# Kernel optimization log

Hardware: AMD Instinct MI355X
Metric: run time of the kernel (lower is better)

## Reference

```python
import jax, jax.numpy as jnp
import numpy as np

N = 20000
T = 6890
FEAT = 128
DEG = 32
K = 6


def setup_inputs() -> dict:
    key = jax.random.key(0)
    k1, k2, k3, k4, k5 = jax.random.split(key, 5)
    source_feats = jax.random.normal(k1, (N, FEAT), dtype=jnp.float32)
    target_feats = jax.random.normal(k2, (T, FEAT), dtype=jnp.float32)
    target_points = jax.random.normal(k3, (T, 3), dtype=jnp.float32)
    pos = jax.random.normal(k4, (N, 3), dtype=jnp.float32)
    # kNN-style graph: every center node (row) has exactly DEG neighbors (col)
    row = jnp.repeat(jnp.arange(N, dtype=jnp.int32), DEG)
    col = jax.random.randint(k5, (N * DEG,), 0, N, dtype=jnp.int32)
    edge_index = jnp.stack([row, col], axis=0)  # [2, E]
    return {"source_feats": source_feats, "target_feats": target_feats,
            "target_points": target_points, "pos": pos, "edge_index": edge_index}


def reference(source_feats, target_feats, target_points, pos, edge_index):
    n = source_feats.shape[0]
    # --- soft retrieval against template ---
    dp = source_feats @ target_feats.T                                 # [N,T]
    dists = ((source_feats * source_feats).sum(-1, keepdims=True)
             - 2.0 * dp
             + (target_feats * target_feats).sum(-1)[None, :])         # [N,T]
    neg_scores, indices = jax.lax.top_k(-dists, K)                      # [N,K]
    scores = jax.nn.softmax(neg_scores, axis=-1)                        # [N,K]
    selected = target_points[indices]                                   # [N,K,3]
    predicted = (selected * scores[..., None]).sum(-2)                  # [N,3]

    row, col = edge_index[0], edge_index[1]
    src_nb = pos[col]                                                   # [E,3]
    tgt_nb = predicted[col]                                             # [E,3]

    cnt = jax.ops.segment_sum(jnp.ones(row.shape, src_nb.dtype), row,
                              num_segments=n)
    cnt = jnp.maximum(cnt, 1.0)[:, None]                                # [N,1]
    src_centers = jax.ops.segment_sum(src_nb, row, num_segments=n) / cnt
    tgt_centers = jax.ops.segment_sum(tgt_nb, row, num_segments=n) / cnt

    sd = src_nb - src_centers[row]                                      # [E,3]
    td = tgt_nb - tgt_centers[row]                                      # [E,3]
    edge_mat = sd[:, :, None] * td[:, None, :]                          # [E,3,3] outer products
    pm = jax.ops.segment_sum(edge_mat, row, num_segments=n)             # [N,3,3]

    # --- Procrustes via batched 3x3 SVD (torch.svd: A = U S V^T; jnp: A = U S Vh => V^T = Vh) ---
    U, S, Vh = jnp.linalg.svd(pm)
    R0 = jax.lax.stop_gradient(U @ Vh)
    detR0 = jnp.linalg.det(R0)
    d = jax.lax.stop_gradient(
        jnp.stack([jnp.ones_like(detR0), jnp.ones_like(detR0), detR0], -1))  # [N,3]
    R = (U * d[:, None, :]) @ Vh                                        # U @ diag(d) @ V^T
    trans = tgt_centers - jnp.einsum('nij,nj->ni', R, src_centers)      # [N,3]

    # --- residual under neighbor transforms ---
    transformed = jnp.einsum('eij,ej->ei', R[col], src_nb) + trans[col]  # [E,3]
    res = transformed - tgt_nb
    dsts = (res * res).sum(-1, keepdims=True)                           # [E,1]
    dst = jax.ops.segment_sum(dsts, row, num_segments=n) / cnt          # [N,1]
    return R, trans, dst
```

## Files before the change

### kernel.cpp

```cpp
#include <hip/hip_runtime.h>
#include <math.h>

#define NS 20000
#define TT 6890
#define TPAD 6912
#define FE 128
#define EDG 640000
#define DEG 32

#define RPB 80
#define NCB 4
#define CBW 1728
#define NH 5

typedef __attribute__((ext_vector_type(8))) short short8;
typedef __attribute__((ext_vector_type(4))) float floatx4;
typedef __attribute__((ext_vector_type(4))) int i32x4;
typedef unsigned int uint;

__device__ __forceinline__ unsigned short f2bf(float f) {
  unsigned int u = __float_as_uint(f);
  return (unsigned short)((u + 0x7fffu + ((u >> 16) & 1u)) >> 16);
}

__device__ __forceinline__ uint med3u(uint a, uint b, uint c) {
  uint d;
  asm("v_med3_u32 %0, %1, %2, %3" : "=v"(d) : "v"(a), "v"(b), "v"(c));
  return d;
}
__device__ __forceinline__ void ins6(uint* a, uint t) {
  a[5] = med3u(a[4], a[5], t);
  a[4] = med3u(a[3], a[4], t);
  a[3] = med3u(a[2], a[3], t);
  a[2] = med3u(a[1], a[2], t);
  a[1] = med3u(a[0], a[1], t);
  a[0] = min(a[0], t);
}
__device__ __forceinline__ void ins12(uint* a, uint t) {
  a[11] = med3u(a[10], a[11], t);
  a[10] = med3u(a[9], a[10], t);
  a[9]  = med3u(a[8], a[9], t);
  a[8]  = med3u(a[7], a[8], t);
  a[7]  = med3u(a[6], a[7], t);
  a[6]  = med3u(a[5], a[6], t);
  a[5]  = med3u(a[4], a[5], t);
  a[4]  = med3u(a[3], a[4], t);
  a[3]  = med3u(a[2], a[3], t);
  a[2]  = med3u(a[1], a[2], t);
  a[1]  = med3u(a[0], a[1], t);
  a[0]  = min(a[0], t);
}

__global__ void tn_cast_kernel(const float* __restrict__ tf, float* __restrict__ tn,
                               float* __restrict__ tn256,
                               unsigned short* __restrict__ tfbx) {
  int gid = blockIdx.x * blockDim.x + threadIdx.x;
  int w = gid >> 6;
  int lane = gid & 63;
  if (w >= TPAD) return;
  unsigned short* base = tfbx + (size_t)w * 128;
  int jj = lane >> 2;
  int soff = ((jj ^ (w & 7)) << 3) + (lane & 3) * 2;
  if (w < TT) {
    const float* p = tf + (size_t)w * FE;
    float a = p[lane];
    float b = p[lane + 64];
    float s = a * a + b * b;
#pragma unroll
    for (int off = 32; off > 0; off >>= 1) s += __shfl_xor(s, off);
    if (lane == 0) { tn[w] = s; tn256[w] = -0.5f * (s + 256.0f); }
    ushort2 o;
    o.x = f2bf(p[2 * lane]);
    o.y = f2bf(p[2 * lane + 1]);
    *reinterpret_cast<ushort2*>(base + soff) = o;
  } else {
    if (lane == 0) { tn[w] = 1e30f; tn256[w] = -1.5e38f; }
    ushort2 z; z.x = 0; z.y = 0;
    *reinterpret_cast<ushort2*>(base + soff) = z;
  }
}

union SmemK1 {
  unsigned short Bs[RPB * 128];
  uint pk[RPB][24];
};

__device__ __forceinline__ void mfma4_sel(
    short8 a0, short8 a1, short8 a2, short8 a3,
    short8 b0, short8 b1, short8 b2, short8 b3,
    float4 t4, uint ck, uint* kqh) {
  floatx4 acc = (floatx4){t4.x, t4.y, t4.z, t4.w};
  acc = __builtin_amdgcn_mfma_f32_16x16x32_bf16(a0, b0, acc, 0, 0, 0);
  acc = __builtin_amdgcn_mfma_f32_16x16x32_bf16(a1, b1, acc, 0, 0, 0);
  acc = __builtin_amdgcn_mfma_f32_16x16x32_bf16(a2, b2, acc, 0, 0, 0);
  acc = __builtin_amdgcn_mfma_f32_16x16x32_bf16(a3, b3, acc, 0, 0, 0);
#pragma unroll
  for (int r = 0; r < 4; ++r) {
    uint t = (__float_as_uint(acc[r]) & 0xFFFFE000u) | (ck + (uint)r);
    ins6(kqh, t);
  }
}

__global__ __launch_bounds__(256, 2) void topk_kernel(
    const float* __restrict__ sf, const unsigned short* __restrict__ tfbx,
    const float* __restrict__ tn256, uint* __restrict__ pkall) {
  __shared__ SmemK1 u;
  const int tid = threadIdx.x;
  const int lane = tid & 63;
  const int wv = tid >> 6;
  const int q = lane >> 4;
  const int m = lane & 15;
  const int rb = (int)blockIdx.x >> 2;
  const int cb = (int)blockIdx.x & 3;
  const int row0 = rb * RPB;
  const int cbase = cb * CBW;

#pragma unroll
  for (int t = 0; t < 5; ++t) {
    int c = tid + t * 256;
    int rr = c >> 4, jj = c & 15;
    const float* src = sf + (size_t)(row0 + rr) * FE + jj * 8;
    float4 f0 = *reinterpret_cast<const float4*>(src);
    float4 f1 = *reinterpret_cast<const float4*>(src + 4);
    union { unsigned short us[8]; uint4 v; } tt;
    tt.us[0] = f2bf(f0.x); tt.us[1] = f2bf(f0.y);
    tt.us[2] = f2bf(f0.z); tt.us[3] = f2bf(f0.w);
    tt.us[4] = f2bf(f1.x); tt.us[5] = f2bf(f1.y);
    tt.us[6] = f2bf(f1.z); tt.us[7] = f2bf(f1.w);
    *reinterpret_cast<uint4*>(u.Bs + rr * 128 + ((jj ^ (rr & 7)) << 3)) = tt.v;
  }

  uint kq[NH][6];
#pragma unroll
  for (int h = 0; h < NH; ++h)
#pragma unroll
    for (int k = 0; k < 6; ++k) kq[h][k] = 0xFFFFFFFFu;

  int rdB[4];
  int aoff[4];
  const int ax = m & 7;
#pragma unroll
  for (int ks = 0; ks < 4; ++ks) {
    int slot = (ks * 4 + q) ^ ax;
    rdB[ks] = m * 128 + (slot << 3);
    aoff[ks] = slot << 3;
  }
  const unsigned short* abase = tfbx + (size_t)(cbase + wv * 16 + m) * 128;
  const uint ck0 = (uint)(cbase + wv * 16 + q * 4);

  __syncthreads();

  short8 bf[NH][4];
  {
    uint bs0 = (uint)(uintptr_t)(&u.Bs[0]);
    uint adr[4];
#pragma unroll
    for (int ks = 0; ks < 4; ++ks) adr[ks] = bs0 + (uint)(rdB[ks] * 2);
#pragma unroll
    for (int h = 0; h < NH; ++h) {
#pragma unroll
      for (int ks = 0; ks < 4; ++ks) {
        union { i32x4 i; short8 s; } t;
        asm volatile("ds_read_b128 %0, %1 offset:%2"
                     : "=v"(t.i) : "v"(adr[ks]), "i"(h * 4096));
        bf[h][ks] = t.s;
      }
    }
    asm volatile("s_waitcnt lgkmcnt(0)" ::: "memory");
    __builtin_amdgcn_sched_barrier(0);
  }

  short8 a0 = *reinterpret_cast<const short8*>(abase + aoff[0]);
  short8 a1 = *reinterpret_cast<const short8*>(abase + aoff[1]);
  short8 a2 = *reinterpret_cast<const short8*>(abase + aoff[2]);
  short8 a3 = *reinterpret_cast<const short8*>(abase + aoff[3]);
  float4 t4 = *reinterpret_cast<const float4*>(tn256 + cbase + wv * 16 + q * 4);

  for (int s = 0; s < 27; ++s) {
    const int sn = (s < 26) ? s + 1 : 26;
    const unsigned short* apn = abase + (size_t)sn * 8192;
    short8 na0 = *reinterpret_cast<const short8*>(apn + aoff[0]);
    short8 na1 = *reinterpret_cast<const short8*>(apn + aoff[1]);
    short8 na2 = *reinterpret_cast<const short8*>(apn + aoff[2]);
    short8 na3 = *reinterpret_cast<const short8*>(apn + aoff[3]);
    float4 nt4 = *reinterpret_cast<const float4*>(
        tn256 + cbase + sn * 64 + wv * 16 + q * 4);
    const uint ck = ck0 + (uint)(s * 64);
#pragma unroll
    for (int h = 0; h < NH; ++h)
      mfma4_sel(a0, a1, a2, a3, bf[h][0], bf[h][1], bf[h][2], bf[h][3],
                t4, ck, kq[h]);
    a0 = na0; a1 = na1; a2 = na2; a3 = na3; t4 = nt4;
  }

#pragma unroll
  for (int h = 0; h < NH; ++h) {
#pragma unroll
    for (int st = 16; st <= 32; st <<= 1) {
      uint inc[6];
#pragma unroll
      for (int k = 0; k < 6; ++k) inc[k] = __shfl_xor(kq[h][k], st);
#pragma unroll
      for (int k = 0; k < 6; ++k) ins6(kq[h], inc[k]);
    }
  }
  __syncthreads();
  if (q == 0) {
#pragma unroll
    for (int h = 0; h < NH; ++h)
#pragma unroll
      for (int k = 0; k < 6; ++k) u.pk[h * 16 + m][wv * 6 + k] = kq[h][k];
  }
  __syncthreads();

  if (tid < RPB) {
    uint md[12];
#pragma unroll
    for (int k = 0; k < 12; ++k) md[k] = 0xFFFFFFFFu;
    for (int j = 0; j < 24; ++j) ins12(md, u.pk[tid][j]);
    uint* dst = pkall + (size_t)(row0 + tid) * 48 + cb * 12;
#pragma unroll
    for (int k = 0; k < 12; ++k) dst[k] = md[k];
  }
}

__global__ __launch_bounds__(256) void merge_kernel(
    const float* __restrict__ sf, const float* __restrict__ tf,
    const float* __restrict__ tn, const uint* __restrict__ pkall,
    const float* __restrict__ tp, float* __restrict__ pred) {
  __shared__ uint  kk[4][24];
  __shared__ float sv[4][24];
  __shared__ int   sc[4][24];
  const int lane = threadIdx.x & 63;
  const int wv = threadIdx.x >> 6;
  const int row = (int)blockIdx.x * 4 + wv;
  uint k0 = 0xFFFFFFFFu;
  if (lane < 48) k0 = pkall[(size_t)row * 48 + lane];
  int r0 = 0;
  for (int j = 0; j < 48; ++j) {
    uint a = __shfl(k0, j);
    r0 += (a < k0) ? 1 : 0;
  }
  if (lane < 48 && r0 < 24) kk[wv][r0] = k0;
  __syncthreads();

  const int g = lane >> 2;
  const int c4 = lane & 3;
  float4 sfc[8];
  const float* srow = sf + (size_t)row * FE;
#pragma unroll
  for (int it = 0; it < 8; ++it)
    sfc[it] = *reinterpret_cast<const float4*>(srow + (it * 4 + c4) * 4);
#pragma unroll
  for (int p = 0; p < 2; ++p) {
    const int j = p * 16 + g;
    if (j < 24) {
      const int col = (int)(kk[wv][j] & 0x1FFFu);
      const float* trow = tf + (size_t)col * FE;
      float acc = 0.f;
#pragma unroll
      for (int it = 0; it < 8; ++it) {
        float4 bv = *reinterpret_cast<const float4*>(trow + (it * 4 + c4) * 4);
        float4 av = sfc[it];
        acc += av.x * bv.x + av.y * bv.y + av.z * bv.z + av.w * bv.w;
      }
      acc += __shfl_xor(acc, 1);
      acc += __shfl_xor(acc, 2);
      if (c4 == 0) {
        sv[wv][j] = tn[col] - 2.f * acc;
        sc[wv][j] = col;
      }
    }
  }
  __syncthreads();
  if (lane == 0) {
    float sd[6]; int sp6[6];
#pragma unroll
    for (int k = 0; k < 6; ++k) { sd[k] = 1e30f; sp6[k] = 0; }
    for (int j = 0; j < 24; ++j) {
      float v = sv[wv][j];
      if (v < sd[5]) {
        sd[5] = v; sp6[5] = j;
#pragma unroll
        for (int k = 4; k >= 0; --k) {
          if (sd[k + 1] < sd[k]) {
            float tvv = sd[k]; sd[k] = sd[k + 1]; sd[k + 1] = tvv;
            int tii = sp6[k]; sp6[k] = sp6[k + 1]; sp6[k + 1] = tii;
          }
        }
      }
    }
    float wgt[6]; float wsum = 0.f;
#pragma unroll
    for (int k = 0; k < 6; ++k) { wgt[k] = __expf(sd[0] - sd[k]); wsum += wgt[k]; }
    float inv = 1.f / wsum;
    float px = 0.f, py = 0.f, pz = 0.f;
#pragma unroll
    for (int k = 0; k < 6; ++k) {
      float scv = wgt[k] * inv;
      const float* qq = tp + (size_t)sc[wv][sp6[k]] * 3;
      px += scv * qq[0]; py += scv * qq[1]; pz += scv * qq[2];
    }
    pred[row * 3 + 0] = px;
    pred[row * 3 + 1] = py;
    pred[row * 3 + 2] = pz;
  }
}

__global__ __launch_bounds__(256) void proc_kernel(
    const int* __restrict__ colp, const float* __restrict__ pos,
    const float* __restrict__ pred, float* __restrict__ Rout,
    float* __restrict__ tout, float* __restrict__ qnorm) {
  int t = blockIdx.x * blockDim.x + threadIdx.x;
  int i = t >> 2;
  int l = t & 3;
  if (i >= NS) return;
  int4 cia[2];
#pragma unroll
  for (int tt = 0; tt < 2; ++tt)
    cia[tt] = reinterpret_cast<const int4*>(colp + (size_t)i * DEG + l * 8)[tt];
  const int* cidx = reinterpret_cast<const int*>(cia);

  double sp[3] = {0, 0, 0}, sq[3] = {0, 0, 0};
  double spq[3][3] = {{0, 0, 0}, {0, 0, 0}, {0, 0, 0}};
#pragma unroll
  for (int e = 0; e < 8; ++e) {
    int c = cidx[e];
    double p0 = pos[c * 3], p1 = pos[c * 3 + 1], p2 = pos[c * 3 + 2];
    double q0 = pred[c * 3], q1 = pred[c * 3 + 1], q2 = pred[c * 3 + 2];
    sp[0] += p0; sp[1] += p1; sp[2] += p2;
    sq[0] += q0; sq[1] += q1; sq[2] += q2;
    spq[0][0] += p0 * q0; spq[0][1] += p0 * q1; spq[0][2] += p0 * q2;
    spq[1][0] += p1 * q0; spq[1][1] += p1 * q1; spq[1][2] += p1 * q2;
    spq[2][0] += p2 * q0; spq[2][1] += p2 * q1; spq[2][2] += p2 * q2;
  }
#pragma unroll
  for (int mask = 1; mask <= 2; mask <<= 1) {
#pragma unroll
    for (int a = 0; a < 3; ++a) {
      sp[a] += __shfl_xor(sp[a], mask);
      sq[a] += __shfl_xor(sq[a], mask);
#pragma unroll
      for (int b = 0; b < 3; ++b) spq[a][b] += __shfl_xor(spq[a][b], mask);
    }
  }

  const double inv = 1.0 / 32.0;
  double A[3][3], sc[3], tcn[3];
  for (int a = 0; a < 3; ++a) {
    sc[a] = sp[a] * inv;
    tcn[a] = sq[a] * inv;
  }
  for (int a = 0; a < 3; ++a)
    for (int b = 0; b < 3; ++b) A[a][b] = spq[a][b] - sp[a] * sq[b] * inv;

  double S[3][3];
  for (int a = 0; a < 3; ++a)
    for (int b = 0; b < 3; ++b)
      S[a][b] = A[0][a] * A[0][b] + A[1][a] * A[1][b] + A[2][a] * A[2][b];
  double V[3][3] = {{1, 0, 0}, {0, 1, 0}, {0, 0, 1}};
  const int JP[3] = {0, 0, 1}, JQ[3] = {1, 2, 2};
  for (int sweep = 0; sweep < 6; ++sweep) {
    for (int r = 0; r < 3; ++r) {
      int p = JP[r], q = JQ[r];
      double apq = S[p][q];
      if (fabs(apq) < 1e-300) continue;
      double theta = (S[q][q] - S[p][p]) / (2.0 * apq);
      double t2 = copysign(1.0 / (fabs(theta) + sqrt(theta * theta + 1.0)), theta);
      double c = 1.0 / sqrt(t2 * t2 + 1.0);
      double s = t2 * c;
      double spp = S[p][p], sqq = S[q][q];
      S[p][p] = spp - t2 * apq;
      S[q][q] = sqq + t2 * apq;
      S[p][q] = 0.0; S[q][p] = 0.0;
      int k = 3 - p - q;
      double skp = S[k][p], skq = S[k][q];
      S[k][p] = S[p][k] = c * skp - s * skq;
      S[k][q] = S[q][k] = s * skp + c * skq;
      for (int mth = 0; mth < 3; ++mth) {
        double vp = V[mth][p], vq = V[mth][q];
        V[mth][p] = c * vp - s * vq;
        V[mth][q] = s * vp + c * vq;
      }
    }
  }
  double lam[3] = {S[0][0], S[1][1], S[2][2]};
  int i0 = 0, i1 = 1, i2 = 2, tmp;
  if (lam[i0] < lam[i1]) { tmp = i0; i0 = i1; i1 = tmp; }
  if (lam[i0] < lam[i2]) { tmp = i0; i0 = i2; i2 = tmp; }
  if (lam[i1] < lam[i2]) { tmp = i1; i1 = i2; i2 = tmp; }
  double v0[3] = {V[0][i0], V[1][i0], V[2][i0]};
  double v1[3] = {V[0][i1], V[1][i1], V[2][i1]};
  double v2[3] = {V[0][i2], V[1][i2], V[2][i2]};

  double Av0[3], Av1[3], Av2[3];
  for (int a = 0; a < 3; ++a) {
    Av0[a] = A[a][0] * v0[0] + A[a][1] * v0[1] + A[a][2] * v0[2];
    Av1[a] = A[a][0] * v1[0] + A[a][1] * v1[1] + A[a][2] * v1[2];
    Av2[a] = A[a][0] * v2[0] + A[a][1] * v2[1] + A[a][2] * v2[2];
  }
  double n0 = fmax(sqrt(Av0[0]*Av0[0] + Av0[1]*Av0[1] + Av0[2]*Av0[2]), 1e-300);
  double u0[3] = {Av0[0] / n0, Av0[1] / n0, Av0[2] / n0};
  double proj = u0[0]*Av1[0] + u0[1]*Av1[1] + u0[2]*Av1[2];
  double u1[3] = {Av1[0] - proj * u0[0], Av1[1] - proj * u0[1], Av1[2] - proj * u0[2]};
  double n1 = fmax(sqrt(u1[0]*u1[0] + u1[1]*u1[1] + u1[2]*u1[2]), 1e-300);
  u1[0] /= n1; u1[1] /= n1; u1[2] /= n1;
  double w[3] = {u0[1]*u1[2] - u0[2]*u1[1],
                 u0[2]*u1[0] - u0[0]*u1[2],
                 u0[0]*u1[1] - u0[1]*u1[0]};
  double dotw = Av2[0]*w[0] + Av2[1]*w[1] + Av2[2]*w[2];
  double sgn = (dotw < 0.0) ? -1.0 : 1.0;
  double detA = A[0][0]*(A[1][1]*A[2][2] - A[1][2]*A[2][1])
              - A[0][1]*(A[1][0]*A[2][2] - A[1][2]*A[2][0])
              + A[0][2]*(A[1][0]*A[2][1] - A[1][1]*A[2][0]);
  double d3 = ((detA < 0.0) ? -1.0 : 1.0) * sgn;

  double R[3][3];
  for (int a = 0; a < 3; ++a)
    for (int b = 0; b < 3; ++b)
      R[a][b] = u0[a]*v0[b] + u1[a]*v1[b] + d3 * w[a]*v2[b];

  if (l == 0) {
    for (int a = 0; a < 3; ++a)
      for (int b = 0; b < 3; ++b) Rout[i * 9 + a * 3 + b] = (float)R[a][b];
    double tr_[3];
    for (int a = 0; a < 3; ++a) {
      tr_[a] = tcn[a] - (R[a][0]*sc[0] + R[a][1]*sc[1] + R[a][2]*sc[2]);
      tout[i * 3 + a] = (float)tr_[a];
    }
    double pxi = pos[i * 3], pyi = pos[i * 3 + 1], pzi = pos[i * 3 + 2];
    double r0 = R[0][0]*pxi + R[0][1]*pyi + R[0][2]*pzi + tr_[0] - pred[i * 3];
    double r1 = R[1][0]*pxi + R[1][1]*pyi + R[1][2]*pzi + tr_[1] - pred[i * 3 + 1];
    double r2 = R[2][0]*pxi + R[2][1]*pyi + R[2][2]*pzi + tr_[2] - pred[i * 3 + 2];
    qnorm[i] = (float)(r0 * r0 + r1 * r1 + r2 * r2);
  }
}

__global__ __launch_bounds__(256) void dst_kernel(
    const int* __restrict__ colp, const float* __restrict__ qn,
    float* __restrict__ dout) {
  int t = blockIdx.x * blockDim.x + threadIdx.x;
  int i = t >> 2;
  int l = t & 3;
  if (i >= NS) return;
  int4 cia[2];
#pragma unroll
  for (int tt = 0; tt < 2; ++tt)
    cia[tt] = reinterpret_cast<const int4*>(colp + (size_t)i * DEG + l * 8)[tt];
  const int* cidx = reinterpret_cast<const int*>(cia);
  float s = 0.f;
#pragma unroll
  for (int e = 0; e < 8; ++e) s += qn[cidx[e]];
  s += __shfl_xor(s, 1);
  s += __shfl_xor(s, 2);
  if (l == 0) dout[i] = s * (1.0f / 32.0f);
}

extern "C" void kernel_launch(void* const* d_in, const int* in_sizes, int n_in,
                              void* d_out, int out_size, void* d_ws, size_t ws_size,
                              hipStream_t stream) {
  const float* sf  = (const float*)d_in[0];
  const float* tf  = (const float*)d_in[1];
  const float* tp  = (const float*)d_in[2];
  const float* pos = (const float*)d_in[3];
  const int*   ei  = (const int*)d_in[4];
  float* out = (float*)d_out;
  char* ws = (char*)d_ws;
  float*          tn    = (float*)(ws);
  float*          tn256 = (float*)(ws + 28672);
  float*          pred  = (float*)(ws + 57344);
  uint*           pkall = (uint*)(ws + 297344);
  unsigned short* tfbx  = (unsigned short*)(ws + 4137344);
  float*          qn    = (float*)(ws + 4137344);
  const int* colp = ei + EDG;

  tn_cast_kernel<<<(TPAD * 64) / 256, 256, 0, stream>>>(tf, tn, tn256, tfbx);
  topk_kernel<<<(NS / RPB) * NCB, 256, 0, stream>>>(sf, tfbx, tn256, pkall);
  merge_kernel<<<NS / 4, 256, 0, stream>>>(sf, tf, tn, pkall, tp, pred);
  proc_kernel<<<(NS * 4 + 255) / 256, 256, 0, stream>>>(colp, pos, pred, out,
                                                        out + NS * 9, qn);
  dst_kernel<<<(NS * 4 + 255) / 256, 256, 0, stream>>>(colp, qn, out + NS * 12);
}
```

Before: 201.9 us.

## Fuse merge into topk via last-block counter and dst into proc via grid barrier

Removes the separate merge and dst kernel launches. The last of the four column blocks for a row band, detected with an atomic counter, performs the exact rescoring and softmax. The proc kernel uses a software grid barrier (spin on an atomic counter) before the neighbor-sum pass. Counters are zeroed in the cast kernel. This saves launch overhead and the gaps between kernels. In exchange, the merge work now runs in only 250 blocks, and the spin barrier depends on all 313 blocks being co-resident.

New measurement: 540.2 us. +167.5%, slower.

```diff
diff --git a/kernel.cpp b/kernel.cpp
--- a/kernel.cpp
+++ b/kernel.cpp
@@ -12,6 +12,7 @@
 #define NCB 4
 #define CBW 1728
 #define NH 5
+#define PBLK 313
 
 typedef __attribute__((ext_vector_type(8))) short short8;
 typedef __attribute__((ext_vector_type(4))) float floatx4;
@@ -53,8 +54,10 @@
 
 __global__ void tn_cast_kernel(const float* __restrict__ tf, float* __restrict__ tn,
                                float* __restrict__ tn256,
-                               unsigned short* __restrict__ tfbx) {
+                               unsigned short* __restrict__ tfbx,
+                               uint* __restrict__ cntp) {
   int gid = blockIdx.x * blockDim.x + threadIdx.x;
+  if (gid < 251) cntp[gid] = 0;
   int w = gid >> 6;
   int lane = gid & 63;
   if (w >= TPAD) return;
@@ -83,12 +86,13 @@
 union SmemK1 {
   unsigned short Bs[RPB * 128];
   uint pk[RPB][24];
+  struct { uint kk[4][24]; float sv[4][24]; int sc[4][24]; } t;
 };
 
 __device__ __forceinline__ void mfma4_sel(
     short8 a0, short8 a1, short8 a2, short8 a3,
     short8 b0, short8 b1, short8 b2, short8 b3,
-    float4 t4, uint ck, uint* kqh) {
+    float4 t4, const uint* ckr, uint* kqh) {
   floatx4 acc = (floatx4){t4.x, t4.y, t4.z, t4.w};
   acc = __builtin_amdgcn_mfma_f32_16x16x32_bf16(a0, b0, acc, 0, 0, 0);
   acc = __builtin_amdgcn_mfma_f32_16x16x32_bf16(a1, b1, acc, 0, 0, 0);
@@ -96,15 +100,19 @@
   acc = __builtin_amdgcn_mfma_f32_16x16x32_bf16(a3, b3, acc, 0, 0, 0);
 #pragma unroll
   for (int r = 0; r < 4; ++r) {
-    uint t = (__float_as_uint(acc[r]) & 0xFFFFE000u) | (ck + (uint)r);
+    uint t = (__float_as_uint(acc[r]) & 0xFFFFE000u) | ckr[r];
     ins6(kqh, t);
   }
 }
 
 __global__ __launch_bounds__(256, 2) void topk_kernel(
-    const float* __restrict__ sf, const unsigned short* __restrict__ tfbx,
-    const float* __restrict__ tn256, uint* __restrict__ pkall) {
+    const float* __restrict__ sf, const float* __restrict__ tf,
+    const unsigned short* __restrict__ tfbx,
+    const float* __restrict__ tn256, const float* __restrict__ tn,
+    const float* __restrict__ tp, uint* __restrict__ pkall,
+    float* __restrict__ pred, uint* __restrict__ cnt) {
   __shared__ SmemK1 u;
+  __shared__ int lastFlag;
   const int tid = threadIdx.x;
   const int lane = tid & 63;
   const int wv = tid >> 6;
@@ -185,11 +193,14 @@
     short8 na3 = *reinterpret_cast<const short8*>(apn + aoff[3]);
     float4 nt4 = *reinterpret_cast<const float4*>(
         tn256 + cbase + sn * 64 + wv * 16 + q * 4);
-    const uint ck = ck0 + (uint)(s * 64);
+    uint ckr[4];
+    const uint cks = ck0 + (uint)(s * 64);
+#pragma unroll
+    for (int r = 0; r < 4; ++r) ckr[r] = cks + (uint)r;
 #pragma unroll
     for (int h = 0; h < NH; ++h)
       mfma4_sel(a0, a1, a2, a3, bf[h][0], bf[h][1], bf[h][2], bf[h][3],
-                t4, ck, kq[h]);
+                t4, ckr, kq[h]);
     a0 = na0; a1 = na1; a2 = na2; a3 = na3; t4 = nt4;
   }
 
@@ -222,103 +233,103 @@
 #pragma unroll
     for (int k = 0; k < 12; ++k) dst[k] = md[k];
   }
-}
-
-__global__ __launch_bounds__(256) void merge_kernel(
-    const float* __restrict__ sf, const float* __restrict__ tf,
-    const float* __restrict__ tn, const uint* __restrict__ pkall,
-    const float* __restrict__ tp, float* __restrict__ pred) {
-  __shared__ uint  kk[4][24];
-  __shared__ float sv[4][24];
-  __shared__ int   sc[4][24];
-  const int lane = threadIdx.x & 63;
-  const int wv = threadIdx.x >> 6;
-  const int row = (int)blockIdx.x * 4 + wv;
-  uint k0 = 0xFFFFFFFFu;
-  if (lane < 48) k0 = pkall[(size_t)row * 48 + lane];
-  int r0 = 0;
-  for (int j = 0; j < 48; ++j) {
-    uint a = __shfl(k0, j);
-    r0 += (a < k0) ? 1 : 0;
-  }
-  if (lane < 48 && r0 < 24) kk[wv][r0] = k0;
-  __syncthreads();
-
-  const int g = lane >> 2;
-  const int c4 = lane & 3;
-  float4 sfc[8];
-  const float* srow = sf + (size_t)row * FE;
-#pragma unroll
-  for (int it = 0; it < 8; ++it)
-    sfc[it] = *reinterpret_cast<const float4*>(srow + (it * 4 + c4) * 4);
-#pragma unroll
-  for (int p = 0; p < 2; ++p) {
-    const int j = p * 16 + g;
-    if (j < 24) {
-      const int col = (int)(kk[wv][j] & 0x1FFFu);
-      const float* trow = tf + (size_t)col * FE;
-      float acc = 0.f;
-#pragma unroll
-      for (int it = 0; it < 8; ++it) {
-        float4 bv = *reinterpret_cast<const float4*>(trow + (it * 4 + c4) * 4);
-        float4 av = sfc[it];
-        acc += av.x * bv.x + av.y * bv.y + av.z * bv.z + av.w * bv.w;
+
+  __syncthreads();
+  if (tid == 0) {
+    __threadfence();
+    lastFlag = (atomicAdd(&cnt[rb], 1u) == 3u) ? 1 : 0;
+  }
+  __syncthreads();
+  if (!lastFlag) return;
+  __threadfence();
+
+  for (int rr = wv; rr < RPB; rr += 4) {
+    const int row = row0 + rr;
+    uint k0 = 0xFFFFFFFFu;
+    if (lane < 48) k0 = pkall[(size_t)row * 48 + lane];
+    int rk = 0;
+    for (int j = 0; j < 48; ++j) {
+      uint a = __shfl(k0, j);
+      rk += (a < k0) ? 1 : 0;
+    }
+    if (lane < 48 && rk < 24) u.t.kk[wv][rk] = k0;
+    const int g = lane >> 2;
+    const int c4 = lane & 3;
+    const float* srow = sf + (size_t)row * FE;
+    float4 sfc[8];
+#pragma unroll
+    for (int it = 0; it < 8; ++it)
+      sfc[it] = *reinterpret_cast<const float4*>(srow + (it * 4 + c4) * 4);
+#pragma unroll
+    for (int p = 0; p < 2; ++p) {
+      const int j = p * 16 + g;
+      if (j < 24) {
+        const int col = (int)(u.t.kk[wv][j] & 0x1FFFu);
+        const float* trow = tf + (size_t)col * FE;
+        float acc = 0.f;
+#pragma unroll
+        for (int it = 0; it < 8; ++it) {
+          float4 bv = *reinterpret_cast<const float4*>(trow + (it * 4 + c4) * 4);
+          float4 av = sfc[it];
+          acc += av.x * bv.x + av.y * bv.y + av.z * bv.z + av.w * bv.w;
+        }
+        acc += __shfl_xor(acc, 1);
+        acc += __shfl_xor(acc, 2);
+        if (c4 == 0) {
+          u.t.sv[wv][j] = tn[col] - 2.f * acc;
+          u.t.sc[wv][j] = col;
+        }
       }
-      acc += __shfl_xor(acc, 1);
-      acc += __shfl_xor(acc, 2);
-      if (c4 == 0) {
-        sv[wv][j] = tn[col] - 2.f * acc;
-        sc[wv][j] = col;
-      }
-    }
-  }
-  __syncthreads();
-  if (lane == 0) {
-    float sd[6]; int sp6[6];
-#pragma unroll
-    for (int k = 0; k < 6; ++k) { sd[k] = 1e30f; sp6[k] = 0; }
-    for (int j = 0; j < 24; ++j) {
-      float v = sv[wv][j];
-      if (v < sd[5]) {
-        sd[5] = v; sp6[5] = j;
-#pragma unroll
-        for (int k = 4; k >= 0; --k) {
-          if (sd[k + 1] < sd[k]) {
-            float tvv = sd[k]; sd[k] = sd[k + 1]; sd[k + 1] = tvv;
-            int tii = sp6[k]; sp6[k] = sp6[k + 1]; sp6[k + 1] = tii;
+    }
+    if (lane == 0) {
+      float sd[6]; int sp6[6];
+#pragma unroll
+      for (int k = 0; k < 6; ++k) { sd[k] = 1e30f; sp6[k] = 0; }
+      for (int j = 0; j < 24; ++j) {
+        float v = u.t.sv[wv][j];
+        if (v < sd[5]) {
+          sd[5] = v; sp6[5] = j;
+#pragma unroll
+          for (int k = 4; k >= 0; --k) {
+            if (sd[k + 1] < sd[k]) {
+              float tvv = sd[k]; sd[k] = sd[k + 1]; sd[k + 1] = tvv;
+              int tii = sp6[k]; sp6[k] = sp6[k + 1]; sp6[k + 1] = tii;
+            }
           }
         }
       }
-    }
-    float wgt[6]; float wsum = 0.f;
-#pragma unroll
-    for (int k = 0; k < 6; ++k) { wgt[k] = __expf(sd[0] - sd[k]); wsum += wgt[k]; }
-    float inv = 1.f / wsum;
-    float px = 0.f, py = 0.f, pz = 0.f;
-#pragma unroll
-    for (int k = 0; k < 6; ++k) {
-      float scv = wgt[k] * inv;
-      const float* qq = tp + (size_t)sc[wv][sp6[k]] * 3;
-      px += scv * qq[0]; py += scv * qq[1]; pz += scv * qq[2];
-    }
-    pred[row * 3 + 0] = px;
-    pred[row * 3 + 1] = py;
-    pred[row * 3 + 2] = pz;
-  }
-}
-
-__global__ __launch_bounds__(256) void proc_kernel(
+      float wgt[6]; float wsum = 0.f;
+#pragma unroll
+      for (int k = 0; k < 6; ++k) { wgt[k] = __expf(sd[0] - sd[k]); wsum += wgt[k]; }
+      float inv = 1.f / wsum;
+      float px = 0.f, py = 0.f, pz = 0.f;
+#pragma unroll
+      for (int k = 0; k < 6; ++k) {
+        float scv = wgt[k] * inv;
+        const float* qq = tp + (size_t)u.t.sc[wv][sp6[k]] * 3;
+        px += scv * qq[0]; py += scv * qq[1]; pz += scv * qq[2];
+      }
+      pred[row * 3 + 0] = px;
+      pred[row * 3 + 1] = py;
+      pred[row * 3 + 2] = pz;
+    }
+  }
+}
+
+__global__ __launch_bounds__(256, 2) void proc_kernel(
     const int* __restrict__ colp, const float* __restrict__ pos,
     const float* __restrict__ pred, float* __restrict__ Rout,
-    float* __restrict__ tout, float* __restrict__ qnorm) {
+    float* __restrict__ tout, float* __restrict__ qnorm,
+    float* __restrict__ dout, uint* __restrict__ cnt2) {
   int t = blockIdx.x * blockDim.x + threadIdx.x;
   int i = t >> 2;
   int l = t & 3;
-  if (i >= NS) return;
+  const bool valid = (i < NS);
+  const int ic = valid ? i : (NS - 1);
   int4 cia[2];
 #pragma unroll
   for (int tt = 0; tt < 2; ++tt)
-    cia[tt] = reinterpret_cast<const int4*>(colp + (size_t)i * DEG + l * 8)[tt];
+    cia[tt] = reinterpret_cast<const int4*>(colp + (size_t)ic * DEG + l * 8)[tt];
   const int* cidx = reinterpret_cast<const int*>(cia);
 
   double sp[3] = {0, 0, 0}, sq[3] = {0, 0, 0};
@@ -420,7 +431,7 @@
     for (int b = 0; b < 3; ++b)
       R[a][b] = u0[a]*v0[b] + u1[a]*v1[b] + d3 * w[a]*v2[b];
 
-  if (l == 0) {
+  if (valid && l == 0) {
     for (int a = 0; a < 3; ++a)
       for (int b = 0; b < 3; ++b) Rout[i * 9 + a * 3 + b] = (float)R[a][b];
     double tr_[3];
@@ -434,26 +445,27 @@
     double r2 = R[2][0]*pxi + R[2][1]*pyi + R[2][2]*pzi + tr_[2] - pred[i * 3 + 2];
     qnorm[i] = (float)(r0 * r0 + r1 * r1 + r2 * r2);
   }
-}
-
-__global__ __launch_bounds__(256) void dst_kernel(
-    const int* __restrict__ colp, const float* __restrict__ qn,
-    float* __restrict__ dout) {
-  int t = blockIdx.x * blockDim.x + threadIdx.x;
-  int i = t >> 2;
-  int l = t & 3;
-  if (i >= NS) return;
-  int4 cia[2];
-#pragma unroll
-  for (int tt = 0; tt < 2; ++tt)
-    cia[tt] = reinterpret_cast<const int4*>(colp + (size_t)i * DEG + l * 8)[tt];
-  const int* cidx = reinterpret_cast<const int*>(cia);
-  float s = 0.f;
-#pragma unroll
-  for (int e = 0; e < 8; ++e) s += qn[cidx[e]];
-  s += __shfl_xor(s, 1);
-  s += __shfl_xor(s, 2);
-  if (l == 0) dout[i] = s * (1.0f / 32.0f);
+
+  __syncthreads();
+  if (threadIdx.x == 0) {
+    __threadfence();
+    atomicAdd(cnt2, 1u);
+    while (__hip_atomic_load(cnt2, __ATOMIC_ACQUIRE, __HIP_MEMORY_SCOPE_AGENT)
+           < (uint)PBLK) {
+      __builtin_amdgcn_s_sleep(2);
+    }
+  }
+  __syncthreads();
+  __threadfence();
+
+  {
+    float s = 0.f;
+#pragma unroll
+    for (int e = 0; e < 8; ++e) s += qnorm[cidx[e]];
+    s += __shfl_xor(s, 1);
+    s += __shfl_xor(s, 2);
+    if (valid && l == 0) dout[i] = s * (1.0f / 32.0f);
+  }
 }
 
 extern "C" void kernel_launch(void* const* d_in, const int* in_sizes, int n_in,
@@ -468,16 +480,16 @@
   char* ws = (char*)d_ws;
   float*          tn    = (float*)(ws);
   float*          tn256 = (float*)(ws + 28672);
+  uint*           cntp  = (uint*)(ws + 56320);
   float*          pred  = (float*)(ws + 57344);
   uint*           pkall = (uint*)(ws + 297344);
   unsigned short* tfbx  = (unsigned short*)(ws + 4137344);
   float*          qn    = (float*)(ws + 4137344);
   const int* colp = ei + EDG;
 
-  tn_cast_kernel<<<(TPAD * 64) / 256, 256, 0, stream>>>(tf, tn, tn256, tfbx);
-  topk_kernel<<<(NS / RPB) * NCB, 256, 0, stream>>>(sf, tfbx, tn256, pkall);
-  merge_kernel<<<NS / 4, 256, 0, stream>>>(sf, tf, tn, pkall, tp, pred);
-  proc_kernel<<<(NS * 4 + 255) / 256, 256, 0, stream>>>(colp, pos, pred, out,
-                                                        out + NS * 9, qn);
-  dst_kernel<<<(NS * 4 + 255) / 256, 256, 0, stream>>>(colp, qn, out + NS * 12);
-}
+  tn_cast_kernel<<<(TPAD * 64) / 256, 256, 0, stream>>>(tf, tn, tn256, tfbx, cntp);
+  topk_kernel<<<(NS / RPB) * NCB, 256, 0, stream>>>(sf, tf, tfbx, tn256, tn, tp,
+                                                    pkall, pred, cntp);
+  proc_kernel<<<PBLK, 256, 0, stream>>>(colp, pos, pred, out, out + NS * 9, qn,
+                                        out + NS * 12, cntp + 250);
+}
```
